# Kernel tuning notes

Measured on AMD Instinct MI355X. Metric: run time of the kernel, lower is better.

Reference implementation:

```python
import jax, jax.numpy as jnp
import numpy as np

D_MODEL = 1024
NUM_HEADS = 16
HEAD_DIM = D_MODEL // NUM_HEADS
THETA = 10000.0


def setup_inputs() -> dict:
    key = jax.random.key(0)
    k1, k2, k3 = jax.random.split(key, 3)
    B, S = 4, 2048
    std_qkv = (2.0 / (D_MODEL + 3 * D_MODEL)) ** 0.5
    std_out = (2.0 / (D_MODEL + D_MODEL)) ** 0.5
    return {
        "x": jax.random.normal(k1, (B, S, D_MODEL), dtype=jnp.float32),
        "token_positions": jnp.arange(S, dtype=jnp.int64 if jax.config.jax_enable_x64 else jnp.int32),
        "w_qkv": jax.random.normal(k2, (3 * D_MODEL, D_MODEL), dtype=jnp.float32) * std_qkv,
        "w_out": jax.random.normal(k3, (D_MODEL, D_MODEL), dtype=jnp.float32) * std_out,
    }


def _apply_rope(x, token_positions):
    # x: [b, h, s, d_h]; token_positions: [s]
    inv_freq = 1.0 / (THETA ** (jnp.arange(0, HEAD_DIM, 2, dtype=jnp.float32) / HEAD_DIM))
    angles = token_positions.astype(jnp.float32)[:, None] * inv_freq  # [s, d_h/2]
    cos, sin = jnp.cos(angles), jnp.sin(angles)
    x_even = x[..., 0::2]
    x_odd = x[..., 1::2]
    out_even = x_even * cos - x_odd * sin
    out_odd = x_even * sin + x_odd * cos
    # re-interleave even/odd lanes
    return jnp.stack([out_even, out_odd], axis=-1).reshape(x.shape)


def reference(x, token_positions, w_qkv, w_out):
    B, S, _ = x.shape
    qkv = jnp.einsum("bsd,ed->bse", x, w_qkv)  # [b, s, 3*d_model]
    q, k, v = jnp.split(qkv, 3, axis=-1)

    def to_heads(t):  # [b, s, d_model] -> [b, h, s, d_h]
        return t.reshape(B, S, NUM_HEADS, HEAD_DIM).transpose(0, 2, 1, 3)

    q, k, v = to_heads(q), to_heads(k), to_heads(v)
    q = _apply_rope(q, token_positions)
    k = _apply_rope(k, token_positions)

    scale = 1.0 / (HEAD_DIM ** 0.5)
    scores = jnp.einsum("bhqd,bhkd->bhqk", q, k) * scale  # [b, h, s, s]
    causal = jnp.tril(jnp.ones((S, S), dtype=bool))
    scores = jnp.where(causal, scores, -jnp.inf)
    probs = jax.nn.softmax(scores, axis=-1)
    out = jnp.einsum("bhqk,bhkd->bhqd", probs, v)  # [b, h, s, d_h]
    out = out.transpose(0, 2, 1, 3).reshape(B, S, D_MODEL)
    return jnp.einsum("bsd,ed->bse", out, w_out)
```

## Files before the change

### kernel.cpp

```cpp
#include <hip/hip_runtime.h>

typedef unsigned short u16;
typedef __attribute__((ext_vector_type(4))) float f32x4;
typedef __attribute__((ext_vector_type(8))) __bf16 bf16x8;
typedef __attribute__((ext_vector_type(8))) short short8;
typedef __attribute__((ext_vector_type(4))) u16 u16x4;

__device__ __forceinline__ u16 f2bf(float f) {
    union { float f; unsigned u; } v; v.f = f;
    unsigned r = v.u + 0x7fffu + ((v.u >> 16) & 1u);
    return (u16)(r >> 16);
}

__device__ __forceinline__ f32x4 mfma16(bf16x8 a, bf16x8 b, f32x4 c) {
    return __builtin_amdgcn_mfma_f32_16x16x32_bf16(a, b, c, 0, 0, 0);
}

__device__ __forceinline__ void gload16(const u16* g, u16* lds) {
    __builtin_amdgcn_global_load_lds(
        (const __attribute__((address_space(1))) void*)g,
        (__attribute__((address_space(3))) void*)lds, 16, 0, 0);
}

__global__ void cvt_bf16_kernel(const float* __restrict__ src, u16* __restrict__ dst, int n4) {
    int i = blockIdx.x * blockDim.x + threadIdx.x;
    if (i >= n4) return;
    float4 v = ((const float4*)src)[i];
    u16x4 o = { f2bf(v.x), f2bf(v.y), f2bf(v.z), f2bf(v.w) };
    *(u16x4*)&dst[i * 4] = o;
}

__global__ void rope_tbl_kernel(const int* __restrict__ pos, float2* __restrict__ tbl) {
    int i = blockIdx.x * blockDim.x + threadIdx.x;
    int s = i >> 5, p = i & 31;
    float inv = powf(10000.0f, -(float)p / 32.0f);
    float a = (float)pos[s] * inv;
    float sn, cs;
    sincosf(a, &sn, &cs);
    tbl[i] = make_float2(cs, sn);
}

template<int MODE>
__global__ __launch_bounds__(256) void gemm_bt(
    const u16* __restrict__ A, const u16* __restrict__ B,
    float* __restrict__ C, int N,
    u16* __restrict__ Qt, u16* __restrict__ Ktn, u16* __restrict__ VTt,
    const float2* __restrict__ tbl)
{
    __shared__ alignas(16) u16 As[128 * 32];
    __shared__ alignas(16) u16 Bs[128 * 32];
    const int t = threadIdx.x;
    const int l = t & 63, w = t >> 6;
    const int lg = l >> 4, lc = l & 15;
    const int wr = w >> 1, wc = w & 1;
    const int brow = blockIdx.y * 128, bcol = blockIdx.x * 128;
    const int sr = w * 16 + (l >> 2), sc = (l & 3) * 8;
    const u16* ga = A + (size_t)(brow + sr) * 1024 + sc;
    const u16* gb = B + (size_t)(bcol + sr) * 1024 + sc;
    u16* la = &As[w * 512];
    u16* lb = &Bs[w * 512];
    f32x4 acc[4][4] = {};

    for (int kt = 0; kt < 1024; kt += 32) {
        __syncthreads();
        gload16(ga + kt, la);
        gload16(ga + 64 * 1024 + kt, la + 2048);
        gload16(gb + kt, lb);
        gload16(gb + 64 * 1024 + kt, lb + 2048);
        __syncthreads();
        bf16x8 af[4], bfr[4];
#pragma unroll
        for (int i = 0; i < 4; ++i)
            af[i] = *(const bf16x8*)&As[(wr * 64 + i * 16 + lc) * 32 + lg * 8];
#pragma unroll
        for (int j = 0; j < 4; ++j)
            bfr[j] = *(const bf16x8*)&Bs[(wc * 64 + j * 16 + lc) * 32 + lg * 8];
#pragma unroll
        for (int i = 0; i < 4; ++i)
#pragma unroll
            for (int j = 0; j < 4; ++j)
                acc[i][j] = mfma16(af[i], bfr[j], acc[i][j]);
    }

    if (MODE == 0) {
#pragma unroll
        for (int i = 0; i < 4; ++i) {
            int row = brow + wr * 64 + i * 16 + lg * 4;
#pragma unroll
            for (int j = 0; j < 4; ++j) {
                int col = bcol + wc * 64 + j * 16 + lc;
#pragma unroll
                for (int jj = 0; jj < 4; ++jj)
                    C[(size_t)(row + jj) * N + col] = acc[i][j][jj];
            }
        }
    } else {
        const int b = brow >> 11;
#pragma unroll
        for (int i = 0; i < 4; ++i) {
            int s0 = (brow & 2047) + wr * 64 + i * 16 + lg * 4;
#pragma unroll
            for (int j = 0; j < 4; ++j) {
                int e0 = bcol + wc * 64 + j * 16;
                int region = e0 >> 10;
                int er = e0 & 1023;
                int h = er >> 6;
                int d = (er & 63) + lc;
                size_t bh = (size_t)(b * 16 + h);
                if (region <= 1) {
                    int p = d >> 1;
                    float sgn = (d & 1) ? 1.0f : -1.0f;
                    u16* dst = (region == 0) ? Qt : Ktn;
                    float mul = (region == 0) ? 0.125f : 1.0f;
#pragma unroll
                    for (int jj = 0; jj < 4; ++jj) {
                        float v = acc[i][j][jj];
                        float pr = __shfl_xor(v, 1);
                        float2 cs = tbl[(size_t)(s0 + jj) * 32 + p];
                        float o = (v * cs.x + pr * cs.y * sgn) * mul;
                        dst[(bh * 2048 + s0 + jj) * 64 + d] = f2bf(o);
                    }
                } else {
                    u16x4 pk;
#pragma unroll
                    for (int jj = 0; jj < 4; ++jj) pk[jj] = f2bf(acc[i][j][jj]);
                    *(u16x4*)&VTt[(bh * 64 + d) * 2048 + s0] = pk;
                }
            }
        }
    }
}

__global__ __launch_bounds__(256) void attn_kernel(
    const u16* __restrict__ Qt, const u16* __restrict__ Kt,
    const u16* __restrict__ VTt, u16* __restrict__ O)
{
    __shared__ alignas(16) u16 Kl[64 * 72];
    __shared__ alignas(16) u16 Vl[64 * 72];
    __shared__ alignas(16) u16 Pl[4 * 16 * 72];
    const int bid = blockIdx.x;
    const int qt = 31 - (bid >> 6);
    const int bh = bid & 63;
    const int t = threadIdx.x, l = t & 63, w = t >> 6;
    const int lg = l >> 4, lc = l & 15;
    const int qw0 = qt * 64 + w * 16;

    const size_t qoff = ((size_t)bh * 2048 + qw0 + lc) * 64 + lg * 8;
    bf16x8 qf[2];
    qf[0] = *(const bf16x8*)&Qt[qoff];
    qf[1] = *(const bf16x8*)&Qt[qoff + 32];

    f32x4 aco[4] = {};
    float m[4], ls[4];
#pragma unroll
    for (int jj = 0; jj < 4; ++jj) { m[jj] = -1e30f; ls[jj] = 0.0f; }

    const int r = t >> 2, cseg = (t & 3) * 16;
    const u16* gK = Kt + (size_t)bh * 2048 * 64;
    const u16* gV = VTt + (size_t)bh * 64 * 2048;

    for (int kt = 0; kt <= qt; ++kt) {
        const int kv0 = kt * 64;
        __syncthreads();
        *(short8*)&Kl[r * 72 + cseg]     = *(const short8*)&gK[(size_t)(kv0 + r) * 64 + cseg];
        *(short8*)&Kl[r * 72 + cseg + 8] = *(const short8*)&gK[(size_t)(kv0 + r) * 64 + cseg + 8];
        *(short8*)&Vl[r * 72 + cseg]     = *(const short8*)&gV[(size_t)r * 2048 + kv0 + cseg];
        *(short8*)&Vl[r * 72 + cseg + 8] = *(const short8*)&gV[(size_t)r * 2048 + kv0 + cseg + 8];
        __syncthreads();

        f32x4 sc[4];
#pragma unroll
        for (int nb = 0; nb < 4; ++nb) {
            sc[nb] = (f32x4){0.f, 0.f, 0.f, 0.f};
#pragma unroll
            for (int fk = 0; fk < 2; ++fk) {
                bf16x8 kb = *(const bf16x8*)&Kl[(nb * 16 + lc) * 72 + fk * 32 + lg * 8];
                sc[nb] = mfma16(qf[fk], kb, sc[nb]);
            }
        }

        float mt[4] = { -1e30f, -1e30f, -1e30f, -1e30f };
#pragma unroll
        for (int nb = 0; nb < 4; ++nb) {
            int kvi = kv0 + nb * 16 + lc;
#pragma unroll
            for (int jj = 0; jj < 4; ++jj) {
                float sv = sc[nb][jj];
                int qi = qw0 + lg * 4 + jj;
                sv = (kvi > qi) ? -1e30f : sv;
                sc[nb][jj] = sv;
                mt[jj] = fmaxf(mt[jj], sv);
            }
        }
#pragma unroll
        for (int jj = 0; jj < 4; ++jj) {
            mt[jj] = fmaxf(mt[jj], __shfl_xor(mt[jj], 1));
            mt[jj] = fmaxf(mt[jj], __shfl_xor(mt[jj], 2));
            mt[jj] = fmaxf(mt[jj], __shfl_xor(mt[jj], 4));
            mt[jj] = fmaxf(mt[jj], __shfl_xor(mt[jj], 8));
        }
        float rs[4] = { 0.f, 0.f, 0.f, 0.f };
#pragma unroll
        for (int jj = 0; jj < 4; ++jj) {
            float mn = fmaxf(m[jj], mt[jj]);
            float scal = __expf(m[jj] - mn);
            m[jj] = mn;
            ls[jj] *= scal;
#pragma unroll
            for (int nb = 0; nb < 4; ++nb) aco[nb][jj] *= scal;
        }
#pragma unroll
        for (int nb = 0; nb < 4; ++nb)
#pragma unroll
            for (int jj = 0; jj < 4; ++jj) {
                float pv = __expf(sc[nb][jj] - m[jj]);
                sc[nb][jj] = pv;
                rs[jj] += pv;
            }
#pragma unroll
        for (int jj = 0; jj < 4; ++jj) {
            rs[jj] += __shfl_xor(rs[jj], 1);
            rs[jj] += __shfl_xor(rs[jj], 2);
            rs[jj] += __shfl_xor(rs[jj], 4);
            rs[jj] += __shfl_xor(rs[jj], 8);
            ls[jj] += rs[jj];
        }

#pragma unroll
        for (int nb = 0; nb < 4; ++nb)
#pragma unroll
            for (int jj = 0; jj < 4; ++jj)
                Pl[w * 1152 + (lg * 4 + jj) * 72 + nb * 16 + lc] = f2bf(sc[nb][jj]);
        __syncthreads();

        bf16x8 pa[2];
        pa[0] = *(const bf16x8*)&Pl[w * 1152 + lc * 72 + lg * 8];
        pa[1] = *(const bf16x8*)&Pl[w * 1152 + lc * 72 + lg * 8 + 32];
#pragma unroll
        for (int nb = 0; nb < 4; ++nb)
#pragma unroll
            for (int fk = 0; fk < 2; ++fk) {
                bf16x8 vb = *(const bf16x8*)&Vl[(nb * 16 + lc) * 72 + fk * 32 + lg * 8];
                aco[nb] = mfma16(pa[fk], vb, aco[nb]);
            }
    }

    const int b = bh >> 4, h = bh & 15;
#pragma unroll
    for (int jj = 0; jj < 4; ++jj) {
        float inv = 1.0f / ls[jj];
        size_t row = (size_t)b * 2048 + qw0 + lg * 4 + jj;
#pragma unroll
        for (int nb = 0; nb < 4; ++nb)
            O[row * 1024 + h * 64 + nb * 16 + lc] = f2bf(aco[nb][jj] * inv);
    }
}

extern "C" void kernel_launch(void* const* d_in, const int* in_sizes, int n_in,
                              void* d_out, int out_size, void* d_ws, size_t ws_size,
                              hipStream_t stream) {
    const float* x    = (const float*)d_in[0];
    const int*   pos  = (const int*)d_in[1];
    const float* wqkv = (const float*)d_in[2];
    const float* wout = (const float*)d_in[3];
    float* out = (float*)d_out;
    char* ws = (char*)d_ws;

    u16*    x_bf    = (u16*)(ws);
    u16*    wqkv_bf = (u16*)(ws + 16777216);
    u16*    wout_bf = (u16*)(ws + 23068672);
    float2* tbl     = (float2*)(ws + 25165824);
    u16*    Qt      = (u16*)(ws + 25690112);
    u16*    Kt      = (u16*)(ws + 42467328);
    u16*    VTt     = (u16*)(ws + 59244544);
    u16*    O       = (u16*)(ws + 76021760);
    if (ws_size < 92798976u) return;

    cvt_bf16_kernel<<<8192, 256, 0, stream>>>(x, x_bf, 2097152);
    cvt_bf16_kernel<<<3072, 256, 0, stream>>>(wqkv, wqkv_bf, 786432);
    cvt_bf16_kernel<<<1024, 256, 0, stream>>>(wout, wout_bf, 262144);
    rope_tbl_kernel<<<256, 256, 0, stream>>>(pos, tbl);

    dim3 g1(24, 64);
    gemm_bt<1><<<g1, 256, 0, stream>>>(x_bf, wqkv_bf, nullptr, 0, Qt, Kt, VTt, tbl);

    attn_kernel<<<2048, 256, 0, stream>>>(Qt, Kt, VTt, O);

    dim3 g2(8, 64);
    gemm_bt<0><<<g2, 256, 0, stream>>>(O, wout_bf, out, 1024, nullptr, nullptr, nullptr, nullptr);
}
```

Before: 329.1 us.

## Rework attention: 128-row Q tiles, transposed MFMA to keep P in registers, lazy rescale

The attention kernel now gives each block 128 query rows (32 per wave), which halves the number of blocks and doubles K/V reuse per LDS load. It computes S^T using K as the A operand so P stays in registers as the B operand of the PV MFMA, removing the Pl LDS round trip and its extra barrier. Q is prescaled by log2(e)/8 so exp2f can be used. Rescaling is skipped unless the running max grows by more than 11, and the next K/V tile is prefetched into registers. The cost is higher register pressure, fewer blocks for occupancy and load balance, and possible precision drift from the lazy rescale threshold.

```diff
diff --git a/kernel.cpp b/kernel.cpp
--- a/kernel.cpp
+++ b/kernel.cpp
@@ -3,6 +3,7 @@
 typedef unsigned short u16;
 typedef __attribute__((ext_vector_type(4))) float f32x4;
 typedef __attribute__((ext_vector_type(8))) __bf16 bf16x8;
+typedef __attribute__((ext_vector_type(4))) __bf16 bf16x4;
 typedef __attribute__((ext_vector_type(8))) short short8;
 typedef __attribute__((ext_vector_type(4))) u16 u16x4;
 
@@ -111,7 +112,7 @@
                     int p = d >> 1;
                     float sgn = (d & 1) ? 1.0f : -1.0f;
                     u16* dst = (region == 0) ? Qt : Ktn;
-                    float mul = (region == 0) ? 0.125f : 1.0f;
+                    float mul = (region == 0) ? 0.18033688011112043f : 1.0f;
 #pragma unroll
                     for (int jj = 0; jj < 4; ++jj) {
                         float v = acc[i][j][jj];
@@ -137,122 +138,161 @@
 {
     __shared__ alignas(16) u16 Kl[64 * 72];
     __shared__ alignas(16) u16 Vl[64 * 72];
-    __shared__ alignas(16) u16 Pl[4 * 16 * 72];
     const int bid = blockIdx.x;
-    const int qt = 31 - (bid >> 6);
+    const int qt = 15 - (bid >> 6);
     const int bh = bid & 63;
     const int t = threadIdx.x, l = t & 63, w = t >> 6;
     const int lg = l >> 4, lc = l & 15;
-    const int qw0 = qt * 64 + w * 16;
-
-    const size_t qoff = ((size_t)bh * 2048 + qw0 + lc) * 64 + lg * 8;
-    bf16x8 qf[2];
-    qf[0] = *(const bf16x8*)&Qt[qoff];
-    qf[1] = *(const bf16x8*)&Qt[qoff + 32];
-
-    f32x4 aco[4] = {};
-    float m[4], ls[4];
-#pragma unroll
-    for (int jj = 0; jj < 4; ++jj) { m[jj] = -1e30f; ls[jj] = 0.0f; }
-
-    const int r = t >> 2, cseg = (t & 3) * 16;
-    const u16* gK = Kt + (size_t)bh * 2048 * 64;
-    const u16* gV = VTt + (size_t)bh * 64 * 2048;
-
-    for (int kt = 0; kt <= qt; ++kt) {
+    const int qb0 = qt * 128 + w * 32;
+
+    bf16x8 qf[2][2];
+#pragma unroll
+    for (int f = 0; f < 2; ++f)
+#pragma unroll
+        for (int fk = 0; fk < 2; ++fk)
+            qf[f][fk] = *(const bf16x8*)&Qt[((size_t)bh * 2048 + qb0 + 16 * f + lc) * 64 + fk * 32 + lg * 8];
+
+    f32x4 aco[2][4] = {};
+    float m[2] = { -1e30f, -1e30f }, ls[2] = { 0.f, 0.f };
+    const int ntiles = 2 * qt + 2;
+
+    const int r = t >> 2, cg = t & 3;
+    const u16* gkp = Kt + (size_t)bh * 131072 + r * 64 + cg * 16;
+    const u16* gvp = VTt + (size_t)bh * 131072 + (size_t)r * 2048 + cg * 16;
+    u16* wk = &Kl[r * 72 + cg * 16];
+    u16* wv = &Vl[r * 72 + cg * 16];
+
+    short8 rk0 = *(const short8*)(gkp);
+    short8 rk1 = *(const short8*)(gkp + 8);
+    short8 rv0 = *(const short8*)(gvp);
+    short8 rv1 = *(const short8*)(gvp + 8);
+
+    for (int kt = 0; kt < ntiles; ++kt) {
         const int kv0 = kt * 64;
         __syncthreads();
-        *(short8*)&Kl[r * 72 + cseg]     = *(const short8*)&gK[(size_t)(kv0 + r) * 64 + cseg];
-        *(short8*)&Kl[r * 72 + cseg + 8] = *(const short8*)&gK[(size_t)(kv0 + r) * 64 + cseg + 8];
-        *(short8*)&Vl[r * 72 + cseg]     = *(const short8*)&gV[(size_t)r * 2048 + kv0 + cseg];
-        *(short8*)&Vl[r * 72 + cseg + 8] = *(const short8*)&gV[(size_t)r * 2048 + kv0 + cseg + 8];
+        *(short8*)wk = rk0; *(short8*)(wk + 8) = rk1;
+        *(short8*)wv = rv0; *(short8*)(wv + 8) = rv1;
+        if (kt + 1 < ntiles) {
+            const int nx = kv0 + 64;
+            rk0 = *(const short8*)(gkp + (size_t)nx * 64);
+            rk1 = *(const short8*)(gkp + (size_t)nx * 64 + 8);
+            rv0 = *(const short8*)(gvp + nx);
+            rv1 = *(const short8*)(gvp + nx + 8);
+        }
         __syncthreads();
 
-        f32x4 sc[4];
+        const int act0 = (kv0 <= qb0 + 15);
+        const int act1 = (kv0 <= qb0 + 31);
+
+        f32x4 sc[2][4];
+        const f32x4 zf = { 0.f, 0.f, 0.f, 0.f };
 #pragma unroll
         for (int nb = 0; nb < 4; ++nb) {
-            sc[nb] = (f32x4){0.f, 0.f, 0.f, 0.f};
+            bf16x8 kb0 = *(const bf16x8*)&Kl[(nb * 16 + lc) * 72 + lg * 8];
+            bf16x8 kb1 = *(const bf16x8*)&Kl[(nb * 16 + lc) * 72 + 32 + lg * 8];
+            if (act0) {
+                sc[0][nb] = mfma16(kb0, qf[0][0], zf);
+                sc[0][nb] = mfma16(kb1, qf[0][1], sc[0][nb]);
+            }
+            if (act1) {
+                sc[1][nb] = mfma16(kb0, qf[1][0], zf);
+                sc[1][nb] = mfma16(kb1, qf[1][1], sc[1][nb]);
+            }
+        }
+
+        float pm[2] = { -1e38f, -1e38f };
+#pragma unroll
+        for (int f = 0; f < 2; ++f) {
+            const int act = f ? act1 : act0;
+            if (!act) continue;
+            const int qq = qb0 + 16 * f + lc;
+            if (kv0 + 63 > qb0 + 16 * f) {
+#pragma unroll
+                for (int nb = 0; nb < 4; ++nb)
+#pragma unroll
+                    for (int jj = 0; jj < 4; ++jj) {
+                        int kk = kv0 + nb * 16 + lg * 4 + jj;
+                        if (kk > qq) sc[f][nb][jj] = -1e38f;
+                    }
+            }
+            float a0 = fmaxf(fmaxf(sc[f][0][0], sc[f][0][1]), fmaxf(sc[f][0][2], sc[f][0][3]));
+            float a1 = fmaxf(fmaxf(sc[f][1][0], sc[f][1][1]), fmaxf(sc[f][1][2], sc[f][1][3]));
+            float a2 = fmaxf(fmaxf(sc[f][2][0], sc[f][2][1]), fmaxf(sc[f][2][2], sc[f][2][3]));
+            float a3 = fmaxf(fmaxf(sc[f][3][0], sc[f][3][1]), fmaxf(sc[f][3][2], sc[f][3][3]));
+            float a = fmaxf(fmaxf(a0, a1), fmaxf(a2, a3));
+            a = fmaxf(a, __shfl_xor(a, 16));
+            a = fmaxf(a, __shfl_xor(a, 32));
+            pm[f] = a;
+        }
+
+        int need = ((act0 && pm[0] > m[0] + 11.0f) || (act1 && pm[1] > m[1] + 11.0f));
+        if (__any(need)) {
+#pragma unroll
+            for (int f = 0; f < 2; ++f) {
+                float mn = fmaxf(m[f], pm[f]);
+                float scal = exp2f(m[f] - mn);
+                m[f] = mn;
+                ls[f] *= scal;
+#pragma unroll
+                for (int nb = 0; nb < 4; ++nb) aco[f][nb] *= scal;
+            }
+        }
+
+        bf16x8 pB[2][2];
+#pragma unroll
+        for (int f = 0; f < 2; ++f) {
+            const int act = f ? act1 : act0;
+            if (!act) continue;
+            float lsf = 0.f;
+#pragma unroll
+            for (int nb = 0; nb < 4; ++nb)
+#pragma unroll
+                for (int jj = 0; jj < 4; ++jj) {
+                    float p = exp2f(sc[f][nb][jj] - m[f]);
+                    sc[f][nb][jj] = p;
+                    lsf += p;
+                }
+            ls[f] += lsf;
 #pragma unroll
             for (int fk = 0; fk < 2; ++fk) {
-                bf16x8 kb = *(const bf16x8*)&Kl[(nb * 16 + lc) * 72 + fk * 32 + lg * 8];
-                sc[nb] = mfma16(qf[fk], kb, sc[nb]);
-            }
-        }
-
-        float mt[4] = { -1e30f, -1e30f, -1e30f, -1e30f };
+                bf16x8 pb;
+#pragma unroll
+                for (int e = 0; e < 4; ++e) {
+                    pb[e]     = (__bf16)sc[f][2 * fk][e];
+                    pb[e + 4] = (__bf16)sc[f][2 * fk + 1][e];
+                }
+                pB[f][fk] = pb;
+            }
+        }
+
 #pragma unroll
         for (int nb = 0; nb < 4; ++nb) {
-            int kvi = kv0 + nb * 16 + lc;
-#pragma unroll
-            for (int jj = 0; jj < 4; ++jj) {
-                float sv = sc[nb][jj];
-                int qi = qw0 + lg * 4 + jj;
-                sv = (kvi > qi) ? -1e30f : sv;
-                sc[nb][jj] = sv;
-                mt[jj] = fmaxf(mt[jj], sv);
-            }
-        }
-#pragma unroll
-        for (int jj = 0; jj < 4; ++jj) {
-            mt[jj] = fmaxf(mt[jj], __shfl_xor(mt[jj], 1));
-            mt[jj] = fmaxf(mt[jj], __shfl_xor(mt[jj], 2));
-            mt[jj] = fmaxf(mt[jj], __shfl_xor(mt[jj], 4));
-            mt[jj] = fmaxf(mt[jj], __shfl_xor(mt[jj], 8));
-        }
-        float rs[4] = { 0.f, 0.f, 0.f, 0.f };
-#pragma unroll
-        for (int jj = 0; jj < 4; ++jj) {
-            float mn = fmaxf(m[jj], mt[jj]);
-            float scal = __expf(m[jj] - mn);
-            m[jj] = mn;
-            ls[jj] *= scal;
-#pragma unroll
-            for (int nb = 0; nb < 4; ++nb) aco[nb][jj] *= scal;
-        }
-#pragma unroll
-        for (int nb = 0; nb < 4; ++nb)
-#pragma unroll
-            for (int jj = 0; jj < 4; ++jj) {
-                float pv = __expf(sc[nb][jj] - m[jj]);
-                sc[nb][jj] = pv;
-                rs[jj] += pv;
-            }
-#pragma unroll
-        for (int jj = 0; jj < 4; ++jj) {
-            rs[jj] += __shfl_xor(rs[jj], 1);
-            rs[jj] += __shfl_xor(rs[jj], 2);
-            rs[jj] += __shfl_xor(rs[jj], 4);
-            rs[jj] += __shfl_xor(rs[jj], 8);
-            ls[jj] += rs[jj];
-        }
-
-#pragma unroll
-        for (int nb = 0; nb < 4; ++nb)
-#pragma unroll
-            for (int jj = 0; jj < 4; ++jj)
-                Pl[w * 1152 + (lg * 4 + jj) * 72 + nb * 16 + lc] = f2bf(sc[nb][jj]);
-        __syncthreads();
-
-        bf16x8 pa[2];
-        pa[0] = *(const bf16x8*)&Pl[w * 1152 + lc * 72 + lg * 8];
-        pa[1] = *(const bf16x8*)&Pl[w * 1152 + lc * 72 + lg * 8 + 32];
-#pragma unroll
-        for (int nb = 0; nb < 4; ++nb)
 #pragma unroll
             for (int fk = 0; fk < 2; ++fk) {
-                bf16x8 vb = *(const bf16x8*)&Vl[(nb * 16 + lc) * 72 + fk * 32 + lg * 8];
-                aco[nb] = mfma16(pa[fk], vb, aco[nb]);
-            }
+                bf16x4 vlo = *(const bf16x4*)&Vl[(nb * 16 + lc) * 72 + fk * 32 + lg * 4];
+                bf16x4 vhi = *(const bf16x4*)&Vl[(nb * 16 + lc) * 72 + fk * 32 + 16 + lg * 4];
+                bf16x8 va = __builtin_shufflevector(vlo, vhi, 0, 1, 2, 3, 4, 5, 6, 7);
+                if (act0) aco[0][nb] = mfma16(va, pB[0][fk], aco[0][nb]);
+                if (act1) aco[1][nb] = mfma16(va, pB[1][fk], aco[1][nb]);
+            }
+        }
     }
 
     const int b = bh >> 4, h = bh & 15;
 #pragma unroll
-    for (int jj = 0; jj < 4; ++jj) {
-        float inv = 1.0f / ls[jj];
-        size_t row = (size_t)b * 2048 + qw0 + lg * 4 + jj;
-#pragma unroll
-        for (int nb = 0; nb < 4; ++nb)
-            O[row * 1024 + h * 64 + nb * 16 + lc] = f2bf(aco[nb][jj] * inv);
+    for (int f = 0; f < 2; ++f) {
+        float s = ls[f];
+        s += __shfl_xor(s, 16);
+        s += __shfl_xor(s, 32);
+        float rinv = 1.0f / s;
+        size_t row = (size_t)b * 2048 + qb0 + 16 * f + lc;
+#pragma unroll
+        for (int nb = 0; nb < 4; ++nb) {
+            u16x4 pk;
+#pragma unroll
+            for (int jj = 0; jj < 4; ++jj) pk[jj] = f2bf(aco[f][nb][jj] * rinv);
+            *(u16x4*)&O[row * 1024 + h * 64 + nb * 16 + lg * 4] = pk;
+        }
     }
 }
 
@@ -284,7 +324,7 @@
     dim3 g1(24, 64);
     gemm_bt<1><<<g1, 256, 0, stream>>>(x_bf, wqkv_bf, nullptr, 0, Qt, Kt, VTt, tbl);
 
-    attn_kernel<<<2048, 256, 0, stream>>>(Qt, Kt, VTt, O);
+    attn_kernel<<<1024, 256, 0, stream>>>(Qt, Kt, VTt, O);
 
     dim3 g2(8, 64);
     gemm_bt<0><<<g2, 256, 0, stream>>>(O, wout_bf, out, 1024, nullptr, nullptr, nullptr, nullptr);
```

After: 309.4 us. 6.0% less time.
